# Kernel tuning notes

Measured on AMD Instinct MI355X. Metric: run time of the kernel, lower is better.

The kernel has to match this reference:

```python
import jax, jax.numpy as jnp
import numpy as np

B, C, H, W = 8, 64, 256, 256
S = 512          # style_dim
K = 3            # modulated conv kernel
LRELU_SLOPE = 0.2
FUSED_SCALE = float(np.sqrt(2.0))
LIN_SCALE = 1.0 / float(np.sqrt(S))          # EqualLinear scale
CONV_SCALE = 1.0 / float(np.sqrt(C * K * K)) # ModulatedConv2d scale


def setup_inputs() -> dict:
    key = jax.random.key(0)
    ks = jax.random.split(key, 8)
    kaiming = float(np.sqrt(2.0 / (C * 9)))  # torch Conv2d default-ish init scale
    return {
        "x": jax.random.normal(ks[0], (B, C, H, W), jnp.float32),
        "style": jax.random.normal(ks[1], (B, S), jnp.float32),
        # bottleneck_IR block 1 (bn=False -> Identity norms, shortcut=identity)
        "w1a": jax.random.normal(ks[2], (C, C, 3, 3), jnp.float32) * kaiming,
        "alpha1": jnp.full((C,), 0.25, jnp.float32),
        "w1b": jax.random.normal(ks[3], (C, C, 3, 3), jnp.float32) * kaiming,
        # bottleneck_IR block 2
        "w2a": jax.random.normal(ks[4], (C, C, 3, 3), jnp.float32) * kaiming,
        "alpha2": jnp.full((C,), 0.25, jnp.float32),
        "w2b": jax.random.normal(ks[5], (C, C, 3, 3), jnp.float32) * kaiming,
        # ModulatedConv2d: EqualLinear(S->C, bias_init=1) + weight [out,in,k,k]
        "mod_w": jax.random.normal(ks[6], (C, S), jnp.float32),
        "mod_b": jnp.ones((C,), jnp.float32),
        "conv_w": jax.random.normal(ks[7], (C, C, K, K), jnp.float32),
        # FusedLeakyReLU bias
        "fused_b": jnp.zeros((C,), jnp.float32),
    }


def _conv3(x, w):
    return jax.lax.conv_general_dilated(
        x, w, (1, 1), "SAME", dimension_numbers=("NCHW", "OIHW", "NCHW"))


def _prelu(x, a):
    return jnp.where(x > 0, x, a[None, :, None, None] * x)


def _bottleneck_ir(x, wa, alpha, wb):
    # shortcut is identity (in_channel==depth, stride=1); norms are Identity (bn=False)
    return x + _conv3(_prelu(_conv3(x, wa), alpha), wb)


def reference(x, style, w1a, alpha1, w1b, w2a, alpha2, w2b,
              mod_w, mod_b, conv_w, fused_b):
    h = _bottleneck_ir(x, w1a, alpha1, w1b)
    h = _bottleneck_ir(h, w2a, alpha2, w2b)

    # ModulatedConv2d (stride 1, no up/down sample, demodulate=True)
    s = style @ (mod_w.T * LIN_SCALE) + mod_b              # [B, Cin]
    w = CONV_SCALE * conv_w[None] * s[:, None, :, None, None]  # [B, Cout, Cin, K, K]
    demod = jax.lax.rsqrt(jnp.sum(w * w, axis=(2, 3, 4)) + 1e-8)
    w = w * demod[:, :, None, None, None]

    Bn, Cin, Hh, Ww = h.shape
    out = jax.lax.conv_general_dilated(
        h.reshape(1, Bn * Cin, Hh, Ww),            # grouped-conv trick
        w.reshape(Bn * C, Cin, K, K),
        (1, 1), "SAME",
        dimension_numbers=("NCHW", "OIHW", "NCHW"),
        feature_group_count=Bn,
    ).reshape(Bn, C, Hh, Ww)

    # FusedLeakyReLU: (x + bias) -> leaky_relu(0.2) -> * sqrt(2)
    ob = out + fused_b[None, :, None, None]
    return jnp.where(ob > 0, ob, LRELU_SLOPE * ob) * FUSED_SCALE
```

## Files before the change

### kernel.cpp

```cpp
#include <hip/hip_runtime.h>
#include <hip/hip_bf16.h>
#include <math.h>

#define BB 8
#define SS 512
#define LIN_SCALE 0.044194173824159216f
#define CONV_SCALE 0.041666666666666664f
#define SQRT2 1.4142135623730951f

typedef __attribute__((ext_vector_type(8))) short short8;
typedef __attribute__((ext_vector_type(16))) float f32x16;

__device__ __forceinline__ ushort bf16h(float v) {
    unsigned u = __float_as_uint(v);
    return (ushort)((u + 0x7fffu + ((u >> 16) & 1u)) >> 16);
}
__device__ __forceinline__ void splitv(float v, ushort& h, ushort& l) {
    h = bf16h(v);
    l = bf16h(v - __uint_as_float((unsigned)h << 16));
}
__device__ __forceinline__ float b2f(ushort u) { return __uint_as_float((unsigned)u << 16); }

__global__ void zero_k(float* z) { z[threadIdx.x] = 0.f; }

__global__ __launch_bounds__(256) void tocl_k(const float* __restrict__ x,
                                              ushort* __restrict__ oH, ushort* __restrict__ oL) {
    __shared__ float tile[64][65];
    const int blk = blockIdx.x;
    const int b = blk >> 10, rem = blk & 1023;
    const int y = rem >> 2, x0 = (rem & 3) << 6;
    const int tid = threadIdx.x, lane = tid & 63, g = tid >> 6;
    const float* xb = x + ((size_t)b << 22) + (y << 8) + x0;
    #pragma unroll
    for (int i = 0; i < 16; ++i) {
        int c = i * 4 + g;
        tile[c][lane] = xb[((size_t)c << 16) + lane];
    }
    __syncthreads();
    const size_t pixbase = ((size_t)b << 16) + (y << 8) + x0;
    #pragma unroll
    for (int i = 0; i < 16; ++i) {
        int xx = i * 4 + g;
        ushort h, l; splitv(tile[lane][xx], h, l);
        size_t idx = (pixbase + xx) * 64 + lane;
        oH[idx] = h; oL[idx] = l;
    }
}

__device__ __forceinline__ void wdecode(int i, int& c, int& tap, int& co, int& ci, int& pl) {
    int e = i & 7;  int t = i >> 3;
    int lh = t & 1; t >>= 1;
    co = t & 63;    t >>= 6;
    pl = t & 1;     t >>= 1;
    int dy = t % 3; t /= 3;
    int dx = t % 3; t /= 3;
    c = t;
    ci = c * 16 + lh * 8 + e;
    tap = dy * 3 + dx;
}

__global__ void packw_k(const float* __restrict__ w, ushort* __restrict__ img) {
    int i = blockIdx.x * 256 + threadIdx.x;
    if (i >= 73728) return;
    int c, tap, co, ci, pl;
    wdecode(i, c, tap, co, ci, pl);
    ushort h, l; splitv(w[(co * 64 + ci) * 9 + tap], h, l);
    img[i] = pl ? l : h;
}

__global__ void style_s_k(const float* __restrict__ style, const float* __restrict__ mod_w,
                          const float* __restrict__ mod_b, float* __restrict__ sbuf) {
    int tid = threadIdx.x;
    int b = tid >> 6, cin = tid & 63;
    float acc = 0.f;
    for (int j = 0; j < SS; ++j) acc += style[b * SS + j] * mod_w[cin * SS + j];
    sbuf[b * 64 + cin] = acc * LIN_SCALE + mod_b[cin];
}

__global__ void demod_k(const float* __restrict__ conv_w, const float* __restrict__ sbuf,
                        float* __restrict__ demod) {
    int tid = threadIdx.x;
    int b = tid >> 6, cout = tid & 63;
    float sum = 0.f;
    for (int cin = 0; cin < 64; ++cin) {
        float m = CONV_SCALE * sbuf[b * 64 + cin];
        const float* wp = conv_w + (cout * 64 + cin) * 9;
        #pragma unroll
        for (int k = 0; k < 9; ++k) { float v = wp[k] * m; sum += v * v; }
    }
    demod[b * 64 + cout] = 1.0f / sqrtf(sum + 1e-8f);
}

__global__ void packmod_k(const float* __restrict__ conv_w, const float* __restrict__ sbuf,
                          const float* __restrict__ demod, ushort* __restrict__ img) {
    int i = blockIdx.x * 256 + threadIdx.x;
    if (i >= 589824) return;
    int b = i / 73728, ii = i % 73728;
    int c, tap, co, ci, pl;
    wdecode(ii, c, tap, co, ci, pl);
    float v = CONV_SCALE * conv_w[(co * 64 + ci) * 9 + tap] * sbuf[b * 64 + ci] * demod[b * 64 + co];
    ushort h, l; splitv(v, h, l);
    img[i] = pl ? l : h;
}

#define GLDS(gsrc, ldst) __builtin_amdgcn_global_load_lds( \
    (const __attribute__((address_space(1))) unsigned int*)(gsrc), \
    (__attribute__((address_space(3))) unsigned int*)(ldst), 16, 0, 0)

#define VWAIT0 asm volatile("s_waitcnt vmcnt(0)" ::: "memory")
#define BAR    __builtin_amdgcn_s_barrier()
#define SCB    __builtin_amdgcn_sched_barrier(0)

template <int EPI, int PERB>
__global__ __launch_bounds__(256, 2)
void mconv_k(const ushort* __restrict__ inH, const ushort* __restrict__ inL,
             const ushort* __restrict__ wimg, const float* __restrict__ aux,
             const ushort* __restrict__ rH, const ushort* __restrict__ rL,
             ushort* __restrict__ oH, ushort* __restrict__ oL,
             float* __restrict__ onchw, const ushort* __restrict__ zb) {
    __shared__ __align__(16) char lds[43520];
    const int tid = threadIdx.x;
    const int orig = blockIdx.x;
    const int blk = (orig & 7) * 256 + (orig >> 3);
    const int b = blk >> 8, t8 = blk & 255;
    const int y0 = (t8 >> 3) << 3, x0 = (t8 & 7) << 5;
    const int wv = tid >> 6, l = tid & 63, ln = l & 31, lh = l >> 5;

    const ushort* wsrc = wimg + (PERB ? (size_t)b * 73728 : 0);

    f32x16 acc[2][2];
    #pragma unroll
    for (int m = 0; m < 2; ++m)
        #pragma unroll
        for (int j = 0; j < 2; ++j) acc[m][j] = (f32x16)(0.0f);

#define ISSUE_DMA(cc, bsel) { \
    const int c0_ = (cc) * 16; \
    char* bufb_ = lds + (bsel) * 21760; \
    _Pragma("unroll") \
    for (int r_ = 0; r_ < 5; ++r_) { \
        int g_ = r_ * 256 + tid; \
        int p_ = g_ >> 2, sp_ = g_ & 3; \
        int s_ = sp_ ^ (p_ & 3); \
        int pl_ = s_ >> 1, kh_ = s_ & 1; \
        int trow_ = p_ >> 5, px_ = p_ & 31; \
        int gy_ = y0 - 1 + trow_; \
        const ushort* base_ = pl_ ? inL : inH; \
        const ushort* src_ = ((unsigned)gy_ < 256u) \
            ? base_ + ((((size_t)b << 16) + ((size_t)gy_ << 8) + (x0 + px_)) << 6) + c0_ + kh_ * 8 \
            : zb; \
        GLDS(src_, bufb_ + r_ * 4096 + (tid & 192) * 16); \
    } \
    if (tid < 80) { \
        int sp_ = tid & 3, q_ = tid >> 2; \
        int trow_ = q_ % 10, side_ = q_ / 10; \
        int s_ = sp_ ^ (trow_ & 3); \
        int pl_ = s_ >> 1, kh_ = s_ & 1; \
        int gy_ = y0 - 1 + trow_; \
        int gx_ = side_ ? x0 + 32 : x0 - 1; \
        const ushort* base_ = pl_ ? inL : inH; \
        const ushort* src_ = (((unsigned)gy_ < 256u) & ((unsigned)gx_ < 256u)) \
            ? base_ + ((((size_t)b << 16) + ((size_t)gy_ << 8) + gx_) << 6) + c0_ + kh_ * 8 \
            : zb; \
        GLDS(src_, bufb_ + 20480 + (tid & 192) * 16); \
    } }

    ISSUE_DMA(0, 0);
    VWAIT0; BAR; SCB;

    #pragma unroll
    for (int c = 0; c < 4; ++c) {
        const char* bufb = lds + (c & 1) * 21760;
        #pragma unroll
        for (int dx = 0; dx < 3; ++dx) {
            short8 aH[3][2], aL[3][2];
            #pragma unroll
            for (int dy = 0; dy < 3; ++dy)
                #pragma unroll
                for (int m = 0; m < 2; ++m) {
                    const ushort* ab = wsrc + (((c * 3 + dx) * 3 + dy) * 2) * 1024
                                       + (m * 32 + ln) * 16 + lh * 8;
                    aH[dy][m] = *(const short8*)ab;
                    aL[dy][m] = *(const short8*)(ab + 1024);
                }
            if (dx == 0 && c < 3) { ISSUE_DMA(c + 1, (c & 1) ^ 1); }

            short8 bH[4], bL[4];
            #pragma unroll
            for (int r = 0; r < 4; ++r) {
                const int trow = 2 * wv + r;
                const int px = ln + dx - 1;
                int offH, offL;
                if (px < 0 || px > 31) {
                    const int side = (px > 31) ? 1 : 0;
                    const int hb = 1280 + (side * 10 + trow) * 4;
                    offH = (hb + (lh ^ (trow & 3))) * 16;
                    offL = (hb + ((2 + lh) ^ (trow & 3))) * 16;
                } else {
                    const int p = trow * 32 + px;
                    offH = (4 * p + (lh ^ (p & 3))) * 16;
                    offL = (4 * p + ((2 + lh) ^ (p & 3))) * 16;
                }
                bH[r] = *(const short8*)(bufb + offH);
                bL[r] = *(const short8*)(bufb + offL);
            }
            #pragma unroll
            for (int dy = 0; dy < 3; ++dy)
                #pragma unroll
                for (int j = 0; j < 2; ++j) {
                    const int r = j + dy;
                    acc[0][j] = __builtin_amdgcn_mfma_f32_32x32x16_bf16(aH[dy][0], bH[r], acc[0][j], 0, 0, 0);
                    acc[0][j] = __builtin_amdgcn_mfma_f32_32x32x16_bf16(aH[dy][0], bL[r], acc[0][j], 0, 0, 0);
                    acc[0][j] = __builtin_amdgcn_mfma_f32_32x32x16_bf16(aL[dy][0], bH[r], acc[0][j], 0, 0, 0);
                    acc[1][j] = __builtin_amdgcn_mfma_f32_32x32x16_bf16(aH[dy][1], bH[r], acc[1][j], 0, 0, 0);
                    acc[1][j] = __builtin_amdgcn_mfma_f32_32x32x16_bf16(aH[dy][1], bL[r], acc[1][j], 0, 0, 0);
                    acc[1][j] = __builtin_amdgcn_mfma_f32_32x32x16_bf16(aL[dy][1], bH[r], acc[1][j], 0, 0, 0);
                }
        }
        if (c < 3) { VWAIT0; SCB; BAR; SCB; }
    }
#undef ISSUE_DMA

    #pragma unroll
    for (int m = 0; m < 2; ++m)
        #pragma unroll
        for (int j = 0; j < 2; ++j) {
            const int yo = y0 + 2 * wv + j;
            const size_t pix = ((size_t)b << 16) + ((size_t)yo << 8) + x0 + ln;
            #pragma unroll
            for (int q = 0; q < 4; ++q) {
                const int co0 = m * 32 + 8 * q + 4 * lh;
                float v0 = acc[m][j][4 * q + 0], v1 = acc[m][j][4 * q + 1];
                float v2 = acc[m][j][4 * q + 2], v3 = acc[m][j][4 * q + 3];
                if (EPI == 0) {
                    float4 al = *(const float4*)(aux + co0);
                    v0 = v0 > 0.f ? v0 : al.x * v0;
                    v1 = v1 > 0.f ? v1 : al.y * v1;
                    v2 = v2 > 0.f ? v2 : al.z * v2;
                    v3 = v3 > 0.f ? v3 : al.w * v3;
                } else if (EPI == 1) {
                    const size_t ca = pix * 64 + co0;
                    ushort4 rh = *(const ushort4*)(rH + ca);
                    ushort4 rl = *(const ushort4*)(rL + ca);
                    v0 += b2f(rh.x) + b2f(rl.x);
                    v1 += b2f(rh.y) + b2f(rl.y);
                    v2 += b2f(rh.z) + b2f(rl.z);
                    v3 += b2f(rh.w) + b2f(rl.w);
                } else {
                    float4 bi = *(const float4*)(aux + co0);
                    float ob;
                    ob = v0 + bi.x; v0 = (ob > 0.f ? ob : 0.2f * ob) * SQRT2;
                    ob = v1 + bi.y; v1 = (ob > 0.f ? ob : 0.2f * ob) * SQRT2;
                    ob = v2 + bi.z; v2 = (ob > 0.f ? ob : 0.2f * ob) * SQRT2;
                    ob = v3 + bi.w; v3 = (ob > 0.f ? ob : 0.2f * ob) * SQRT2;
                }
                if (EPI == 2) {
                    const size_t sp = ((size_t)yo << 8) + x0 + ln;
                    onchw[(((size_t)(b * 64 + co0 + 0)) << 16) + sp] = v0;
                    onchw[(((size_t)(b * 64 + co0 + 1)) << 16) + sp] = v1;
                    onchw[(((size_t)(b * 64 + co0 + 2)) << 16) + sp] = v2;
                    onchw[(((size_t)(b * 64 + co0 + 3)) << 16) + sp] = v3;
                } else {
                    ushort4 h4, l4;
                    splitv(v0, h4.x, l4.x); splitv(v1, h4.y, l4.y);
                    splitv(v2, h4.z, l4.z); splitv(v3, h4.w, l4.w);
                    const size_t ca = pix * 64 + co0;
                    *(ushort4*)(oH + ca) = h4;
                    *(ushort4*)(oL + ca) = l4;
                }
            }
        }
}

extern "C" void kernel_launch(void* const* d_in, const int* in_sizes, int n_in,
                              void* d_out, int out_size, void* d_ws, size_t ws_size,
                              hipStream_t stream) {
    const float* x       = (const float*)d_in[0];
    const float* style   = (const float*)d_in[1];
    const float* w1a     = (const float*)d_in[2];
    const float* alpha1  = (const float*)d_in[3];
    const float* w1b     = (const float*)d_in[4];
    const float* w2a     = (const float*)d_in[5];
    const float* alpha2  = (const float*)d_in[6];
    const float* w2b     = (const float*)d_in[7];
    const float* mod_w   = (const float*)d_in[8];
    const float* mod_b   = (const float*)d_in[9];
    const float* conv_w  = (const float*)d_in[10];
    const float* fused_b = (const float*)d_in[11];
    float* out = (float*)d_out;

    char* ws = (char*)d_ws;
    float*  zbf   = (float*)ws;
    float*  sbuf  = (float*)(ws + 256);
    float*  demod = (float*)(ws + 2304);
    ushort* wfix  = (ushort*)(ws + 4352);
    ushort* wmod  = (ushort*)(ws + 594176);
    char*   pl    = ws + 1774080;
    const size_t PAIRB = 134217728ull;
    const size_t PLEL  = 33554432ull;

    ushort* XPH = (ushort*)pl;             ushort* XPL = XPH + PLEL;
    ushort* PBH = (ushort*)(pl + PAIRB);   ushort* PBL = PBH + PLEL;
    ushort *PAH, *PAL;
    if (ws_size >= 1774080ull + 3 * PAIRB) {
        PAH = (ushort*)(pl + 2 * PAIRB); PAL = PAH + PLEL;
    } else {
        PAH = (ushort*)d_out; PAL = PAH + PLEL;
    }
    const ushort* zb = (const ushort*)zbf;

    hipLaunchKernelGGL(zero_k, dim3(1), dim3(64), 0, stream, zbf);
    hipLaunchKernelGGL(tocl_k, dim3(BB * 1024), dim3(256), 0, stream, x, XPH, XPL);
    hipLaunchKernelGGL(packw_k, dim3(288), dim3(256), 0, stream, w1a, wfix + 0 * 73728);
    hipLaunchKernelGGL(packw_k, dim3(288), dim3(256), 0, stream, w1b, wfix + 1 * 73728);
    hipLaunchKernelGGL(packw_k, dim3(288), dim3(256), 0, stream, w2a, wfix + 2 * 73728);
    hipLaunchKernelGGL(packw_k, dim3(288), dim3(256), 0, stream, w2b, wfix + 3 * 73728);
    hipLaunchKernelGGL(style_s_k, dim3(1), dim3(512), 0, stream, style, mod_w, mod_b, sbuf);
    hipLaunchKernelGGL(demod_k, dim3(1), dim3(512), 0, stream, conv_w, sbuf, demod);
    hipLaunchKernelGGL(packmod_k, dim3(2304), dim3(256), 0, stream, conv_w, sbuf, demod, wmod);

    const dim3 cgrid(2048), cblk(256);
    hipLaunchKernelGGL((mconv_k<0, 0>), cgrid, cblk, 0, stream,
        XPH, XPL, wfix + 0 * 73728, alpha1, (const ushort*)nullptr, (const ushort*)nullptr,
        PAH, PAL, (float*)nullptr, zb);
    hipLaunchKernelGGL((mconv_k<1, 0>), cgrid, cblk, 0, stream,
        PAH, PAL, wfix + 1 * 73728, (const float*)nullptr, XPH, XPL,
        PBH, PBL, (float*)nullptr, zb);
    hipLaunchKernelGGL((mconv_k<0, 0>), cgrid, cblk, 0, stream,
        PBH, PBL, wfix + 2 * 73728, alpha2, (const ushort*)nullptr, (const ushort*)nullptr,
        PAH, PAL, (float*)nullptr, zb);
    hipLaunchKernelGGL((mconv_k<1, 0>), cgrid, cblk, 0, stream,
        PAH, PAL, wfix + 3 * 73728, (const float*)nullptr, PBH, PBL,
        PBH, PBL, (float*)nullptr, zb);
    hipLaunchKernelGGL((mconv_k<2, 1>), cgrid, cblk, 0, stream,
        PBH, PBL, wmod, fused_b, (const ushort*)nullptr, (const ushort*)nullptr,
        (ushort*)nullptr, (ushort*)nullptr, out, zb);
}
```

Before: 929.2 us.

## Double-buffer weight fragments in registers and relax vmcnt waits in mconv pipeline

Restructures the modulated conv main loop into 12 explicit phases. Weight (A) fragments for the next phase are loaded into a second register bank while the current phase's MFMAs run. DMA source addresses are precomputed once per thread, and the LDS swizzle changes from XOR to a rotate form. Barrier waits use vmcnt(12) instead of vmcnt(0), so the 12 in-flight weight loads need not drain before the barrier, and MFMA sections are wrapped in s_setprio. The cost is higher register pressure from two A banks, which may hurt occupancy at launch_bounds(256,2). It also relies on counter ordering being correct for the LDS DMA.

```diff
diff --git a/kernel.cpp b/kernel.cpp
--- a/kernel.cpp
+++ b/kernel.cpp
@@ -107,9 +107,9 @@
     (const __attribute__((address_space(1))) unsigned int*)(gsrc), \
     (__attribute__((address_space(3))) unsigned int*)(ldst), 16, 0, 0)
 
-#define VWAIT0 asm volatile("s_waitcnt vmcnt(0)" ::: "memory")
-#define BAR    __builtin_amdgcn_s_barrier()
-#define SCB    __builtin_amdgcn_sched_barrier(0)
+#define VWAIT12 asm volatile("s_waitcnt vmcnt(12)" ::: "memory")
+#define BAR     __builtin_amdgcn_s_barrier()
+#define SCB     __builtin_amdgcn_sched_barrier(0)
 
 template <int EPI, int PERB>
 __global__ __launch_bounds__(256, 2)
@@ -127,6 +127,34 @@
     const int wv = tid >> 6, l = tid & 63, ln = l & 31, lh = l >> 5;
 
     const ushort* wsrc = wimg + (PERB ? (size_t)b * 73728 : 0);
+    const int aoff = ln * 16 + lh * 8;
+
+    const ushort* iaddr[5];
+    #pragma unroll
+    for (int r = 0; r < 5; ++r) {
+        int G = r * 256 + tid;
+        int p = G >> 2, sp = G & 3;
+        int k = (sp - (p >> 1)) & 3;
+        int pl_ = k >> 1, kh = k & 1;
+        int trow = p >> 5, px = p & 31;
+        int gy = y0 - 1 + trow;
+        const ushort* base = pl_ ? inL : inH;
+        iaddr[r] = ((unsigned)gy < 256u)
+            ? base + ((((size_t)b << 16) + ((size_t)gy << 8) + (x0 + px)) << 6) + kh * 8
+            : zb;
+    }
+    const ushort* haddr = zb;
+    if (tid < 80) {
+        int q = tid >> 2, sp = tid & 3;
+        int k = (sp - (q >> 1)) & 3;
+        int pl_ = k >> 1, kh = k & 1;
+        int side = q / 10, trow = q % 10;
+        int gy = y0 - 1 + trow;
+        int gx = side ? x0 + 32 : x0 - 1;
+        const ushort* base = pl_ ? inL : inH;
+        if (((unsigned)gy < 256u) & ((unsigned)gx < 256u))
+            haddr = base + ((((size_t)b << 16) + ((size_t)gy << 8) + gx) << 6) + kh * 8;
+    }
 
     f32x16 acc[2][2];
     #pragma unroll
@@ -134,92 +162,67 @@
         #pragma unroll
         for (int j = 0; j < 2; ++j) acc[m][j] = (f32x16)(0.0f);
 
+    short8 A0H[3][2], A0L[3][2], A1H[3][2], A1L[3][2];
+
 #define ISSUE_DMA(cc, bsel) { \
-    const int c0_ = (cc) * 16; \
     char* bufb_ = lds + (bsel) * 21760; \
-    _Pragma("unroll") \
-    for (int r_ = 0; r_ < 5; ++r_) { \
-        int g_ = r_ * 256 + tid; \
-        int p_ = g_ >> 2, sp_ = g_ & 3; \
-        int s_ = sp_ ^ (p_ & 3); \
-        int pl_ = s_ >> 1, kh_ = s_ & 1; \
-        int trow_ = p_ >> 5, px_ = p_ & 31; \
-        int gy_ = y0 - 1 + trow_; \
-        const ushort* base_ = pl_ ? inL : inH; \
-        const ushort* src_ = ((unsigned)gy_ < 256u) \
-            ? base_ + ((((size_t)b << 16) + ((size_t)gy_ << 8) + (x0 + px_)) << 6) + c0_ + kh_ * 8 \
-            : zb; \
-        GLDS(src_, bufb_ + r_ * 4096 + (tid & 192) * 16); \
+    _Pragma("unroll") for (int r_ = 0; r_ < 5; ++r_) \
+        GLDS(iaddr[r_] + (cc) * 16, bufb_ + r_ * 4096 + (tid & 192) * 16); \
+    if (tid < 80) GLDS(haddr + (cc) * 16, bufb_ + 20480 + (tid & 192) * 16); }
+
+#define LOADA(BNK, PH) { \
+    _Pragma("unroll") for (int dy_ = 0; dy_ < 3; ++dy_) { \
+        const ushort* ab_ = wsrc + (size_t)((PH) * 3 + dy_) * 2048 + aoff; \
+        BNK##H[dy_][0] = *(const short8*)ab_; \
+        BNK##H[dy_][1] = *(const short8*)(ab_ + 512); \
+        BNK##L[dy_][0] = *(const short8*)(ab_ + 1024); \
+        BNK##L[dy_][1] = *(const short8*)(ab_ + 1536); \
+    } }
+
+#define PHASE(I, C, DX, CURB, NXTB) { \
+    if ((I) < 11) LOADA(NXTB, (I) + 1); \
+    if ((DX) == 0 && (C) < 3) ISSUE_DMA((C) + 1, ((C) + 1) & 1); \
+    const char* bufb_ = lds + ((C) & 1) * 21760; \
+    short8 bH[4], bL[4]; \
+    _Pragma("unroll") for (int r_ = 0; r_ < 4; ++r_) { \
+        const int trow_ = 2 * wv + r_; \
+        const int px_ = ln + (DX) - 1; \
+        const int p_ = trow_ * 32 + px_; \
+        const int q_ = ((px_ > 31) ? 10 : 0) + trow_; \
+        const bool hal_ = (px_ < 0) | (px_ > 31); \
+        const int gH_ = hal_ ? (1280 + 4 * q_ + ((lh + (q_ >> 1)) & 3)) \
+                             : (4 * p_ + ((lh + (p_ >> 1)) & 3)); \
+        const int gL_ = hal_ ? (1280 + 4 * q_ + ((2 + lh + (q_ >> 1)) & 3)) \
+                             : (4 * p_ + ((2 + lh + (p_ >> 1)) & 3)); \
+        bH[r_] = *(const short8*)(bufb_ + gH_ * 16); \
+        bL[r_] = *(const short8*)(bufb_ + gL_ * 16); \
     } \
-    if (tid < 80) { \
-        int sp_ = tid & 3, q_ = tid >> 2; \
-        int trow_ = q_ % 10, side_ = q_ / 10; \
-        int s_ = sp_ ^ (trow_ & 3); \
-        int pl_ = s_ >> 1, kh_ = s_ & 1; \
-        int gy_ = y0 - 1 + trow_; \
-        int gx_ = side_ ? x0 + 32 : x0 - 1; \
-        const ushort* base_ = pl_ ? inL : inH; \
-        const ushort* src_ = (((unsigned)gy_ < 256u) & ((unsigned)gx_ < 256u)) \
-            ? base_ + ((((size_t)b << 16) + ((size_t)gy_ << 8) + gx_) << 6) + c0_ + kh_ * 8 \
-            : zb; \
-        GLDS(src_, bufb_ + 20480 + (tid & 192) * 16); \
-    } }
+    __builtin_amdgcn_s_setprio(1); \
+    _Pragma("unroll") for (int dy_ = 0; dy_ < 3; ++dy_) \
+        _Pragma("unroll") for (int j_ = 0; j_ < 2; ++j_) { \
+            const int r_ = j_ + dy_; \
+            acc[0][j_] = __builtin_amdgcn_mfma_f32_32x32x16_bf16(CURB##H[dy_][0], bH[r_], acc[0][j_], 0, 0, 0); \
+            acc[0][j_] = __builtin_amdgcn_mfma_f32_32x32x16_bf16(CURB##H[dy_][0], bL[r_], acc[0][j_], 0, 0, 0); \
+            acc[0][j_] = __builtin_amdgcn_mfma_f32_32x32x16_bf16(CURB##L[dy_][0], bH[r_], acc[0][j_], 0, 0, 0); \
+            acc[1][j_] = __builtin_amdgcn_mfma_f32_32x32x16_bf16(CURB##H[dy_][1], bH[r_], acc[1][j_], 0, 0, 0); \
+            acc[1][j_] = __builtin_amdgcn_mfma_f32_32x32x16_bf16(CURB##H[dy_][1], bL[r_], acc[1][j_], 0, 0, 0); \
+            acc[1][j_] = __builtin_amdgcn_mfma_f32_32x32x16_bf16(CURB##L[dy_][1], bH[r_], acc[1][j_], 0, 0, 0); \
+        } \
+    __builtin_amdgcn_s_setprio(0); \
+    if ((DX) == 2 && (C) < 3) { SCB; VWAIT12; BAR; SCB; } }
 
     ISSUE_DMA(0, 0);
-    VWAIT0; BAR; SCB;
-
-    #pragma unroll
-    for (int c = 0; c < 4; ++c) {
-        const char* bufb = lds + (c & 1) * 21760;
-        #pragma unroll
-        for (int dx = 0; dx < 3; ++dx) {
-            short8 aH[3][2], aL[3][2];
-            #pragma unroll
-            for (int dy = 0; dy < 3; ++dy)
-                #pragma unroll
-                for (int m = 0; m < 2; ++m) {
-                    const ushort* ab = wsrc + (((c * 3 + dx) * 3 + dy) * 2) * 1024
-                                       + (m * 32 + ln) * 16 + lh * 8;
-                    aH[dy][m] = *(const short8*)ab;
-                    aL[dy][m] = *(const short8*)(ab + 1024);
-                }
-            if (dx == 0 && c < 3) { ISSUE_DMA(c + 1, (c & 1) ^ 1); }
-
-            short8 bH[4], bL[4];
-            #pragma unroll
-            for (int r = 0; r < 4; ++r) {
-                const int trow = 2 * wv + r;
-                const int px = ln + dx - 1;
-                int offH, offL;
-                if (px < 0 || px > 31) {
-                    const int side = (px > 31) ? 1 : 0;
-                    const int hb = 1280 + (side * 10 + trow) * 4;
-                    offH = (hb + (lh ^ (trow & 3))) * 16;
-                    offL = (hb + ((2 + lh) ^ (trow & 3))) * 16;
-                } else {
-                    const int p = trow * 32 + px;
-                    offH = (4 * p + (lh ^ (p & 3))) * 16;
-                    offL = (4 * p + ((2 + lh) ^ (p & 3))) * 16;
-                }
-                bH[r] = *(const short8*)(bufb + offH);
-                bL[r] = *(const short8*)(bufb + offL);
-            }
-            #pragma unroll
-            for (int dy = 0; dy < 3; ++dy)
-                #pragma unroll
-                for (int j = 0; j < 2; ++j) {
-                    const int r = j + dy;
-                    acc[0][j] = __builtin_amdgcn_mfma_f32_32x32x16_bf16(aH[dy][0], bH[r], acc[0][j], 0, 0, 0);
-                    acc[0][j] = __builtin_amdgcn_mfma_f32_32x32x16_bf16(aH[dy][0], bL[r], acc[0][j], 0, 0, 0);
-                    acc[0][j] = __builtin_amdgcn_mfma_f32_32x32x16_bf16(aL[dy][0], bH[r], acc[0][j], 0, 0, 0);
-                    acc[1][j] = __builtin_amdgcn_mfma_f32_32x32x16_bf16(aH[dy][1], bH[r], acc[1][j], 0, 0, 0);
-                    acc[1][j] = __builtin_amdgcn_mfma_f32_32x32x16_bf16(aH[dy][1], bL[r], acc[1][j], 0, 0, 0);
-                    acc[1][j] = __builtin_amdgcn_mfma_f32_32x32x16_bf16(aL[dy][1], bH[r], acc[1][j], 0, 0, 0);
-                }
-        }
-        if (c < 3) { VWAIT0; SCB; BAR; SCB; }
-    }
+    LOADA(A0, 0);
+    SCB; VWAIT12; BAR; SCB;
+
+    PHASE(0, 0, 0, A0, A1);  PHASE(1, 0, 1, A1, A0);  PHASE(2, 0, 2, A0, A1);
+    PHASE(3, 1, 0, A1, A0);  PHASE(4, 1, 1, A0, A1);  PHASE(5, 1, 2, A1, A0);
+    PHASE(6, 2, 0, A0, A1);  PHASE(7, 2, 1, A1, A0);  PHASE(8, 2, 2, A0, A1);
+    PHASE(9, 3, 0, A1, A0);  PHASE(10, 3, 1, A0, A1); PHASE(11, 3, 2, A1, A0);
+
 #undef ISSUE_DMA
+#undef LOADA
+#undef PHASE
 
     #pragma unroll
     for (int m = 0; m < 2; ++m)
```

New measurement: 1.116 ms. 20.1% more time.
